# Performance work log

Measured on AMD Instinct MI355X. Metric: run time of the kernel, lower is better.

## Reference

```python
import jax, jax.numpy as jnp
import numpy as np

B, S, D, H = 4, 2048, 1024, 16
DH = D // H  # head dim = 64
MASK_VALUE = -1000000.0


def setup_inputs() -> dict:
    key = jax.random.key(0)
    ks = jax.random.split(key, 8)
    return {
        "key": jax.random.normal(ks[0], (B, S, D), jnp.float32),
        "query": jax.random.normal(ks[1], (B, S, D), jnp.float32),
        "value": jax.random.normal(ks[2], (B, S, D), jnp.float32),
        "valid_lens": jax.random.randint(ks[3], (B,), 0, 2048, jnp.int32),
        # nn.Linear weights stored as [out_features, in_features]
        "Wk": jax.random.normal(ks[4], (D, D), jnp.float32) / np.sqrt(D),
        "Wq": jax.random.normal(ks[5], (D, D), jnp.float32) / np.sqrt(D),
        "Wv": jax.random.normal(ks[6], (D, D), jnp.float32) / np.sqrt(D),
        "Wo": jax.random.normal(ks[7], (D, D), jnp.float32) / np.sqrt(D),
    }


def _split_heads(x):
    # [B, S, D] -> [B, H, S, DH]
    return x.reshape(B, S, H, DH).transpose(0, 2, 1, 3)


def reference(key, query, value, valid_lens, Wk, Wq, Wv, Wo):
    # projections (Linear: x @ W^T, bias=False)
    q = _split_heads(query @ Wq.T)  # [B, H, S, DH]
    k = _split_heads(key @ Wk.T)
    v = _split_heads(value @ Wv.T)

    scale = 1.0 / jnp.sqrt(jnp.asarray(DH, q.dtype))
    scores = jnp.einsum("bhqd,bhkd->bhqk", q, k) * scale  # [B, H, S, S]

    # valid_lens masks the key axis per batch element (same for all heads/queries)
    key_mask = jnp.arange(S) < valid_lens[:, None]  # [B, S]
    scores = jnp.where(key_mask[:, None, None, :], scores, MASK_VALUE)

    attn = jax.nn.softmax(scores, axis=-1)
    out = jnp.einsum("bhqk,bhkd->bhqd", attn, v)  # [B, H, S, DH]
    out = out.transpose(0, 2, 1, 3).reshape(B, S, D)  # concat heads
    return out @ Wo.T
```

## Files before the change

kernel.cpp:

```cpp
#include <hip/hip_runtime.h>
#include <hip/hip_bf16.h>
#include <stdint.h>

typedef __bf16 bf16;
typedef __bf16 bf16x4 __attribute__((ext_vector_type(4)));
typedef __bf16 bf16x8 __attribute__((ext_vector_type(8)));
typedef float f32x4 __attribute__((ext_vector_type(4)));
typedef float f32x8 __attribute__((ext_vector_type(8)));

#define MFMA16 __builtin_amdgcn_mfma_f32_16x16x32_bf16

__device__ __forceinline__ void gload_lds16(void* lds, const void* g) {
  __builtin_amdgcn_global_load_lds(
      (const __attribute__((address_space(1))) unsigned int*)g,
      (__attribute__((address_space(3))) unsigned int*)lds, 16, 0, 0);
}

__global__ __launch_bounds__(256) void cvt3(
    const float* __restrict__ s0, const float* __restrict__ s1,
    const float* __restrict__ s2, bf16* __restrict__ d0,
    bf16* __restrict__ d1, bf16* __restrict__ d2) {
  const float* srcs[3] = {s0, s1, s2};
  bf16* dsts[3] = {d0, d1, d2};
  const float* src = srcs[blockIdx.y];
  bf16* dst = dsts[blockIdx.y];
  int i = (blockIdx.x * 256 + threadIdx.x) * 4;
  f32x4 v = *(const f32x4*)(src + i);
  bf16x4 o;
#pragma unroll
  for (int j = 0; j < 4; j++) o[j] = (bf16)v[j];
  *(bf16x4*)(dst + i) = o;
}

__global__ __launch_bounds__(256) void cvt1(const float* __restrict__ src,
                                            bf16* __restrict__ dst) {
  int i = (blockIdx.x * 256 + threadIdx.x) * 4;
  f32x4 v = *(const f32x4*)(src + i);
  bf16x4 o;
#pragma unroll
  for (int j = 0; j < 4; j++) o[j] = (bf16)v[j];
  *(bf16x4*)(dst + i) = o;
}

__global__ __launch_bounds__(256) void cvt4(const float* __restrict__ w0,
                                            const float* __restrict__ w1,
                                            const float* __restrict__ w2,
                                            const float* __restrict__ w3,
                                            bf16* __restrict__ dst) {
  const float* srcs[4] = {w0, w1, w2, w3};
  const float* src = srcs[blockIdx.y];
  int i = (blockIdx.x * 256 + threadIdx.x) * 4;
  f32x4 v = *(const f32x4*)(src + i);
  bf16x4 o;
#pragma unroll
  for (int j = 0; j < 4; j++) o[j] = (bf16)v[j];
  *(bf16x4*)(dst + (size_t)blockIdx.y * 1048576 + i) = o;
}

__device__ __forceinline__ void xcd_remap(int& m0, int& n0) {
  int id = blockIdx.y * 8 + blockIdx.x;
  int xcd = id & 7;
  int j = id >> 3;
  m0 = (xcd * 8 + (j >> 3)) * 128;
  n0 = (j & 7) * 128;
}

__device__ __forceinline__ void gemm_body(const bf16* __restrict__ A,
                                          const bf16* __restrict__ W,
                                          void* __restrict__ Craw, int mode,
                                          int m0, int n0, bf16* As, bf16* Bs) {
  constexpr int K = 1024;
  const int t = threadIdx.x;
  const int lane = t & 63;
  const int quad = lane >> 4;
  const int m16 = lane & 15;
  const int w = t >> 6;
  const int wm = (w >> 1) * 64;
  const int wn = (w & 1) * 64;

  f32x4 acc[4][4];
#pragma unroll
  for (int i = 0; i < 4; i++)
#pragma unroll
    for (int j = 0; j < 4; j++) acc[i][j] = (f32x4){0.f, 0.f, 0.f, 0.f};

  for (int kt = 0; kt < K / 32; kt++) {
    __syncthreads();
#pragma unroll
    for (int p = 0; p < 2; p++) {
      int idx = p * 256 + t;
      int row = idx >> 2;
      int ce = (idx & 3) * 8;
      gload_lds16(&As[idx * 8], A + (size_t)(m0 + row) * K + kt * 32 + ce);
      gload_lds16(&Bs[idx * 8], W + (size_t)(n0 + row) * K + kt * 32 + ce);
    }
    __syncthreads();

    bf16x8 af[4], bfr[4];
#pragma unroll
    for (int i = 0; i < 4; i++) {
      af[i] = *(const bf16x8*)&As[(wm + i * 16 + m16) * 32 + quad * 8];
      bfr[i] = *(const bf16x8*)&Bs[(wn + i * 16 + m16) * 32 + quad * 8];
    }
#pragma unroll
    for (int i = 0; i < 4; i++)
#pragma unroll
      for (int j = 0; j < 4; j++)
        acc[i][j] = MFMA16(af[i], bfr[j], acc[i][j], 0, 0, 0);
  }

#pragma unroll
  for (int i = 0; i < 4; i++) {
    int rbase = m0 + wm + i * 16 + quad * 4;
#pragma unroll
    for (int j = 0; j < 4; j++) {
      int col = n0 + wn + j * 16 + m16;
#pragma unroll
      for (int r = 0; r < 4; r++) {
        int row = rbase + r;
        if (mode == 0) {
          ((float*)Craw)[(size_t)row * 1024 + col] = acc[i][j][r];
        } else {
          int b = row >> 11, s = row & 2047;
          int h = col >> 6, d = col & 63;
          bf16 v = (bf16)acc[i][j][r];
          if (mode == 1)
            ((bf16*)Craw)[(((size_t)(b * 16 + h)) * 2048 + s) * 64 + d] = v;
          else
            ((bf16*)Craw)[(((size_t)(b * 16 + h)) * 64 + d) * 2048 + s] = v;
        }
      }
    }
  }
}

__global__ __launch_bounds__(256) void gemm_qkv(
    const bf16* __restrict__ xq, const bf16* __restrict__ xk,
    const bf16* __restrict__ xv, const bf16* __restrict__ wb,
    const int* __restrict__ vlen, bf16* __restrict__ qp,
    bf16* __restrict__ kp, bf16* __restrict__ vt) {
  __shared__ bf16 As[128 * 32];
  __shared__ bf16 Bs[128 * 32];
  int m0, n0;
  xcd_remap(m0, n0);
  const int z = blockIdx.z;
  if (z >= 1) {
    int b = m0 >> 11;
    int s0 = m0 & 2047;
    int vl = vlen[b];
    if (vl != 0 && s0 >= vl) return;
  }
  const bf16* A = (z == 0) ? xq : (z == 1) ? xk : xv;
  const bf16* W = wb + (size_t)z * 1048576;
  bf16* C = (z == 0) ? qp : (z == 1) ? kp : vt;
  gemm_body(A, W, C, (z == 2) ? 2 : 1, m0, n0, As, Bs);
}

__global__ __launch_bounds__(256) void gemm_one(const bf16* __restrict__ A,
                                                const bf16* __restrict__ W,
                                                void* __restrict__ Craw,
                                                int mode) {
  __shared__ bf16 As[128 * 32];
  __shared__ bf16 Bs[128 * 32];
  int m0, n0;
  xcd_remap(m0, n0);
  gemm_body(A, W, Craw, mode, m0, n0, As, Bs);
}

template <int AF32, int WF32>
__global__ __launch_bounds__(256) void gemm_bt(const void* __restrict__ Araw,
                                               const void* __restrict__ Wraw,
                                               void* __restrict__ Craw,
                                               int mode) {
  constexpr int K = 1024;
  __shared__ bf16 As[128 * 32];
  __shared__ bf16 Bs[128 * 32];
  const int t = threadIdx.x;
  const int lane = t & 63;
  const int quad = lane >> 4;
  const int m16 = lane & 15;
  const int w = t >> 6;
  const int m0 = blockIdx.y * 128;
  const int n0 = blockIdx.x * 128;
  const int wm = (w >> 1) * 64;
  const int wn = (w & 1) * 64;

  f32x4 acc[4][4];
#pragma unroll
  for (int i = 0; i < 4; i++)
#pragma unroll
    for (int j = 0; j < 4; j++) acc[i][j] = (f32x4){0.f, 0.f, 0.f, 0.f};

  for (int kt = 0; kt < K / 32; kt++) {
    bf16x8 aR[2], bR[2];
#pragma unroll
    for (int p = 0; p < 2; p++) {
      int idx = p * 256 + t;
      int row = idx >> 2;
      int ce = (idx & 3) * 8;
      size_t aoff = (size_t)(m0 + row) * K + kt * 32 + ce;
      size_t boff = (size_t)(n0 + row) * K + kt * 32 + ce;
      if constexpr (AF32) {
        f32x8 av = *(const f32x8*)((const float*)Araw + aoff);
#pragma unroll
        for (int j = 0; j < 8; j++) aR[p][j] = (bf16)av[j];
      } else {
        aR[p] = *(const bf16x8*)((const bf16*)Araw + aoff);
      }
      if constexpr (WF32) {
        f32x8 bv = *(const f32x8*)((const float*)Wraw + boff);
#pragma unroll
        for (int j = 0; j < 8; j++) bR[p][j] = (bf16)bv[j];
      } else {
        bR[p] = *(const bf16x8*)((const bf16*)Wraw + boff);
      }
    }
    __syncthreads();
#pragma unroll
    for (int p = 0; p < 2; p++) {
      int idx = p * 256 + t;
      *(bf16x8*)&As[idx * 8] = aR[p];
      *(bf16x8*)&Bs[idx * 8] = bR[p];
    }
    __syncthreads();

    bf16x8 af[4], bfr[4];
#pragma unroll
    for (int i = 0; i < 4; i++) {
      af[i] = *(const bf16x8*)&As[(wm + i * 16 + m16) * 32 + quad * 8];
      bfr[i] = *(const bf16x8*)&Bs[(wn + i * 16 + m16) * 32 + quad * 8];
    }
#pragma unroll
    for (int i = 0; i < 4; i++)
#pragma unroll
      for (int j = 0; j < 4; j++)
        acc[i][j] = MFMA16(af[i], bfr[j], acc[i][j], 0, 0, 0);
  }

#pragma unroll
  for (int i = 0; i < 4; i++) {
    int rbase = m0 + wm + i * 16 + quad * 4;
#pragma unroll
    for (int j = 0; j < 4; j++) {
      int col = n0 + wn + j * 16 + m16;
#pragma unroll
      for (int r = 0; r < 4; r++) {
        int row = rbase + r;
        if (mode == 0) {
          ((float*)Craw)[(size_t)row * 1024 + col] = acc[i][j][r];
        } else {
          int b = row >> 11, s = row & 2047;
          int h = col >> 6, d = col & 63;
          bf16 v = (bf16)acc[i][j][r];
          if (mode == 1)
            ((bf16*)Craw)[(((size_t)(b * 16 + h)) * 2048 + s) * 64 + d] = v;
          else
            ((bf16*)Craw)[(((size_t)(b * 16 + h)) * 64 + d) * 2048 + s] = v;
        }
      }
    }
  }
}

__global__ __launch_bounds__(256) void attn(const bf16* __restrict__ qp,
                                            const bf16* __restrict__ kp,
                                            const bf16* __restrict__ vt,
                                            const int* __restrict__ vlen,
                                            bf16* __restrict__ ctx) {
  __shared__ bf16 Ks[64 * 64];
  __shared__ bf16 Vs[64 * 64];
  __shared__ bf16 Ps[4 * 32 * 72];

  const int t = threadIdx.x;
  const int lane = t & 63;
  const int quad = lane >> 4;
  const int m16 = lane & 15;
  const int sw = m16 & 7;
  const int w = t >> 6;
  const int bh = blockIdx.y;
  const int qt = blockIdx.x;
  const int b = bh >> 4;
  const int h = bh & 15;
  const int vl = vlen[b];

  const float C1 = 0.18033688f;
  const float C2 = 46.166241f;
  const float mArg = (vl == 0) ? 0.0f : -12800.0f;

  bf16x8 qf[2][2];
#pragma unroll
  for (int a = 0; a < 2; a++) {
    const bf16* qb =
        qp + ((size_t)(bh * 2048 + qt * 128 + w * 32 + a * 16 + m16)) * 64;
    qf[a][0] = *(const bf16x8*)(qb + quad * 8);
    qf[a][1] = *(const bf16x8*)(qb + 32 + quad * 8);
  }

  float rsum[2][4] = {{0.f, 0.f, 0.f, 0.f}, {0.f, 0.f, 0.f, 0.f}};
  f32x4 o[2][4];
#pragma unroll
  for (int a = 0; a < 2; a++)
#pragma unroll
    for (int nt = 0; nt < 4; nt++) o[a][nt] = (f32x4){0.f, 0.f, 0.f, 0.f};

  const int ktEnd = (vl == 0) ? 32 : ((vl + 63) >> 6);

  for (int kt = 0; kt < ktEnd; kt++) {
    __syncthreads();
#pragma unroll
    for (int p = 0; p < 2; p++) {
      int idx = p * 256 + t;
      int row = idx >> 3;
      int gc = (idx & 7) ^ (row & 7);
      gload_lds16(&Ks[idx * 8],
                  &kp[((size_t)(bh * 2048 + kt * 64 + row)) * 64 + gc * 8]);
      gload_lds16(&Vs[idx * 8],
                  &vt[((size_t)(bh * 64 + row)) * 2048 + kt * 64 + gc * 8]);
    }
    __syncthreads();

    f32x4 s[2][4];
#pragma unroll
    for (int a = 0; a < 2; a++)
#pragma unroll
      for (int nt = 0; nt < 4; nt++) s[a][nt] = (f32x4){0.f, 0.f, 0.f, 0.f};
#pragma unroll
    for (int nt = 0; nt < 4; nt++) {
      int key = nt * 16 + m16;
#pragma unroll
      for (int ks = 0; ks < 2; ks++) {
        bf16x8 kf =
            *(const bf16x8*)&Ks[key * 64 + (((ks * 4 + quad) ^ sw) * 8)];
        s[0][nt] = MFMA16(qf[0][ks], kf, s[0][nt], 0, 0, 0);
        s[1][nt] = MFMA16(qf[1][ks], kf, s[1][nt], 0, 0, 0);
      }
    }

#pragma unroll
    for (int nt = 0; nt < 4; nt++) {
      bool masked = (kt * 64 + nt * 16 + m16) >= vl;
#pragma unroll
      for (int a = 0; a < 2; a++)
#pragma unroll
        for (int r = 0; r < 4; r++) {
          float arg = masked ? mArg : (s[a][nt][r] * C1 - C2);
          bf16 pb = (bf16)__builtin_amdgcn_exp2f(arg);
          rsum[a][r] += (float)pb;
          Ps[w * 2304 + (a * 16 + quad * 4 + r) * 72 + nt * 16 + m16] = pb;
        }
    }

#pragma unroll
    for (int ks = 0; ks < 2; ks++) {
      bf16x8 pf0 = *(const bf16x8*)&Ps[w * 2304 + m16 * 72 + ks * 32 + quad * 8];
      bf16x8 pf1 =
          *(const bf16x8*)&Ps[w * 2304 + (16 + m16) * 72 + ks * 32 + quad * 8];
#pragma unroll
      for (int nt = 0; nt < 4; nt++) {
        int dh = nt * 16 + m16;
        bf16x8 vf =
            *(const bf16x8*)&Vs[dh * 64 + (((ks * 4 + quad) ^ sw) * 8)];
        o[0][nt] = MFMA16(pf0, vf, o[0][nt], 0, 0, 0);
        o[1][nt] = MFMA16(pf1, vf, o[1][nt], 0, 0, 0);
      }
    }
  }

#pragma unroll
  for (int off = 1; off < 16; off <<= 1)
#pragma unroll
    for (int a = 0; a < 2; a++)
#pragma unroll
      for (int r = 0; r < 4; r++) rsum[a][r] += __shfl_xor(rsum[a][r], off);
#pragma unroll
  for (int a = 0; a < 2; a++)
#pragma unroll
    for (int r = 0; r < 4; r++) rsum[a][r] = 1.0f / rsum[a][r];

#pragma unroll
  for (int a = 0; a < 2; a++)
#pragma unroll
    for (int nt = 0; nt < 4; nt++) {
      int dh = nt * 16 + m16;
#pragma unroll
      for (int r = 0; r < 4; r++) {
        int srow = qt * 128 + w * 32 + a * 16 + quad * 4 + r;
        ctx[((size_t)(b * 2048 + srow)) * 1024 + h * 64 + dh] =
            (bf16)(o[a][nt][r] * rsum[a][r]);
      }
    }
}

extern "C" void kernel_launch(void* const* d_in, const int* in_sizes, int n_in,
                              void* d_out, int out_size, void* d_ws,
                              size_t ws_size, hipStream_t stream) {
  const float* key = (const float*)d_in[0];
  const float* query = (const float*)d_in[1];
  const float* value = (const float*)d_in[2];
  const int* vlen = (const int*)d_in[3];
  const float* Wk = (const float*)d_in[4];
  const float* Wq = (const float*)d_in[5];
  const float* Wv = (const float*)d_in[6];
  const float* Wo = (const float*)d_in[7];

  const size_t NE = (size_t)4 * 2048 * 1024;
  const size_t WE = 1048576;

  const size_t needA = (6 * NE + 4 * WE) * sizeof(bf16);
  const size_t needB = (5 * NE + 4 * WE) * sizeof(bf16);
  dim3 gg(8, 64), gb(256);

  if (ws_size >= needA) {
    bf16* qp = (bf16*)d_ws;
    bf16* kp = qp + NE;
    bf16* vt = kp + NE;
    bf16* xq = vt + NE;
    bf16* xk = xq + NE;
    bf16* xv = xk + NE;
    bf16* wb = xv + NE;
    bf16* ctx = xq;

    cvt4<<<dim3(1024, 4), gb, 0, stream>>>(Wq, Wk, Wv, Wo, wb);
    cvt3<<<dim3(8192, 3), gb, 0, stream>>>(query, key, value, xq, xk, xv);
    gemm_qkv<<<dim3(8, 64, 3), gb, 0, stream>>>(xq, xk, xv, wb, vlen, qp, kp,
                                                vt);
    attn<<<dim3(16, 64), gb, 0, stream>>>(qp, kp, vt, vlen, ctx);
    gemm_one<<<gg, gb, 0, stream>>>(ctx, wb + 3 * WE, d_out, 0);
  } else if (ws_size >= needB) {
    bf16* qp = (bf16*)d_ws;
    bf16* kp = qp + NE;
    bf16* vt = kp + NE;
    bf16* ctx = vt + NE;
    bf16* xb = ctx + NE;
    bf16* wb = xb + NE;

    cvt4<<<dim3(1024, 4), gb, 0, stream>>>(Wq, Wk, Wv, Wo, wb);
    cvt1<<<8192, gb, 0, stream>>>(query, xb);
    gemm_one<<<gg, gb, 0, stream>>>(xb, wb + 0 * WE, qp, 1);
    cvt1<<<8192, gb, 0, stream>>>(key, xb);
    gemm_one<<<gg, gb, 0, stream>>>(xb, wb + 1 * WE, kp, 1);
    cvt1<<<8192, gb, 0, stream>>>(value, xb);
    gemm_one<<<gg, gb, 0, stream>>>(xb, wb + 2 * WE, vt, 2);
    attn<<<dim3(16, 64), gb, 0, stream>>>(qp, kp, vt, vlen, ctx);
    gemm_one<<<gg, gb, 0, stream>>>(ctx, wb + 3 * WE, d_out, 0);
  } else {
    bf16* qp = (bf16*)d_ws;
    bf16* kp = qp + NE;
    bf16* vt = kp + NE;
    bf16* ctx = vt + NE;
    gemm_bt<1, 1><<<gg, gb, 0, stream>>>(query, Wq, qp, 1);
    gemm_bt<1, 1><<<gg, gb, 0, stream>>>(key, Wk, kp, 1);
    gemm_bt<1, 1><<<gg, gb, 0, stream>>>(value, Wv, vt, 2);
    attn<<<dim3(16, 64), gb, 0, stream>>>(qp, kp, vt, vlen, ctx);
    gemm_bt<0, 1><<<gg, gb, 0, stream>>>(ctx, Wo, d_out, 0);
  }
}
```

Baseline: 335.4 us.

## Fuse fp32-to-bf16 input conversion into QKV GEMM and retile output projection

The separate cvt3 pass over the three activation tensors is removed. The QKV GEMM now loads fp32 activations straight into XOR-swizzled LDS and converts them to bf16 while building MFMA fragments, which saves a full read-write round trip of the inputs. The output projection gets its own kernel with 128x64 tiles, twice as many blocks, and a different XCD remapping that changes which tiles share an XCD. The trade-offs are twice the LDS per block and extra conversion ALU work inside the GEMM inner loop, and the needB fallback path is dropped.

```diff
diff --git a/kernel.cpp b/kernel.cpp
--- a/kernel.cpp
+++ b/kernel.cpp
@@ -14,32 +14,6 @@
   __builtin_amdgcn_global_load_lds(
       (const __attribute__((address_space(1))) unsigned int*)g,
       (__attribute__((address_space(3))) unsigned int*)lds, 16, 0, 0);
-}
-
-__global__ __launch_bounds__(256) void cvt3(
-    const float* __restrict__ s0, const float* __restrict__ s1,
-    const float* __restrict__ s2, bf16* __restrict__ d0,
-    bf16* __restrict__ d1, bf16* __restrict__ d2) {
-  const float* srcs[3] = {s0, s1, s2};
-  bf16* dsts[3] = {d0, d1, d2};
-  const float* src = srcs[blockIdx.y];
-  bf16* dst = dsts[blockIdx.y];
-  int i = (blockIdx.x * 256 + threadIdx.x) * 4;
-  f32x4 v = *(const f32x4*)(src + i);
-  bf16x4 o;
-#pragma unroll
-  for (int j = 0; j < 4; j++) o[j] = (bf16)v[j];
-  *(bf16x4*)(dst + i) = o;
-}
-
-__global__ __launch_bounds__(256) void cvt1(const float* __restrict__ src,
-                                            bf16* __restrict__ dst) {
-  int i = (blockIdx.x * 256 + threadIdx.x) * 4;
-  f32x4 v = *(const f32x4*)(src + i);
-  bf16x4 o;
-#pragma unroll
-  for (int j = 0; j < 4; j++) o[j] = (bf16)v[j];
-  *(bf16x4*)(dst + i) = o;
 }
 
 __global__ __launch_bounds__(256) void cvt4(const float* __restrict__ w0,
@@ -57,19 +31,41 @@
   *(bf16x4*)(dst + (size_t)blockIdx.y * 1048576 + i) = o;
 }
 
-__device__ __forceinline__ void xcd_remap(int& m0, int& n0) {
+__device__ __forceinline__ void remap8(int& m0, int& n0) {
   int id = blockIdx.y * 8 + blockIdx.x;
   int xcd = id & 7;
   int j = id >> 3;
-  m0 = (xcd * 8 + (j >> 3)) * 128;
+  m0 = ((j >> 3) * 8 + xcd) * 128;
   n0 = (j & 7) * 128;
 }
 
-__device__ __forceinline__ void gemm_body(const bf16* __restrict__ A,
-                                          const bf16* __restrict__ W,
-                                          void* __restrict__ Craw, int mode,
-                                          int m0, int n0, bf16* As, bf16* Bs) {
-  constexpr int K = 1024;
+__device__ __forceinline__ void remap16(int& m0, int& n0) {
+  int id = blockIdx.y * 16 + blockIdx.x;
+  int xcd = id & 7;
+  int j = id >> 3;
+  m0 = ((j >> 4) * 8 + xcd) * 128;
+  n0 = (j & 15) * 64;
+}
+
+__global__ __launch_bounds__(256) void gemm_qkv(
+    const float* __restrict__ q, const float* __restrict__ k,
+    const float* __restrict__ v, const bf16* __restrict__ wb,
+    const int* __restrict__ vlen, bf16* __restrict__ qp,
+    bf16* __restrict__ kp, bf16* __restrict__ vt) {
+  __shared__ float Asf[128 * 32];
+  __shared__ bf16 Bs[128 * 32];
+  int m0, n0;
+  remap8(m0, n0);
+  const int z = blockIdx.z;
+  if (z >= 1) {
+    int b = m0 >> 11, s0 = m0 & 2047, vl = vlen[b];
+    if (vl != 0 && s0 >= vl) return;
+  }
+  const float* A = (z == 0) ? q : (z == 1) ? k : v;
+  const bf16* W = wb + (size_t)z * 1048576;
+  bf16* C = (z == 0) ? qp : (z == 1) ? kp : vt;
+  const int mode = (z == 2) ? 2 : 1;
+
   const int t = threadIdx.x;
   const int lane = t & 63;
   const int quad = lane >> 4;
@@ -84,22 +80,40 @@
 #pragma unroll
     for (int j = 0; j < 4; j++) acc[i][j] = (f32x4){0.f, 0.f, 0.f, 0.f};
 
-  for (int kt = 0; kt < K / 32; kt++) {
-    __syncthreads();
+  for (int kt = 0; kt < 32; kt++) {
+    __syncthreads();
+#pragma unroll
+    for (int p = 0; p < 4; p++) {
+      int idx = p * 256 + t;
+      int row = idx >> 3;
+      int gc = (idx & 7) ^ (row & 7);
+      gload_lds16(&Asf[idx * 4],
+                  A + (size_t)(m0 + row) * 1024 + kt * 32 + gc * 4);
+    }
 #pragma unroll
     for (int p = 0; p < 2; p++) {
       int idx = p * 256 + t;
       int row = idx >> 2;
       int ce = (idx & 3) * 8;
-      gload_lds16(&As[idx * 8], A + (size_t)(m0 + row) * K + kt * 32 + ce);
-      gload_lds16(&Bs[idx * 8], W + (size_t)(n0 + row) * K + kt * 32 + ce);
+      gload_lds16(&Bs[idx * 8],
+                  W + (size_t)(n0 + row) * 1024 + kt * 32 + ce);
     }
     __syncthreads();
 
     bf16x8 af[4], bfr[4];
 #pragma unroll
     for (int i = 0; i < 4; i++) {
-      af[i] = *(const bf16x8*)&As[(wm + i * 16 + m16) * 32 + quad * 8];
+      int rr = wm + i * 16 + m16;
+      int e = rr & 7;
+      f32x4 lo = *(const f32x4*)&Asf[rr * 32 + (((2 * quad) ^ e) * 4)];
+      f32x4 hi = *(const f32x4*)&Asf[rr * 32 + (((2 * quad + 1) ^ e) * 4)];
+      bf16x8 a8;
+#pragma unroll
+      for (int j = 0; j < 4; j++) {
+        a8[j] = (bf16)lo[j];
+        a8[4 + j] = (bf16)hi[j];
+      }
+      af[i] = a8;
       bfr[i] = *(const bf16x8*)&Bs[(wn + i * 16 + m16) * 32 + quad * 8];
     }
 #pragma unroll
@@ -118,53 +132,84 @@
 #pragma unroll
       for (int r = 0; r < 4; r++) {
         int row = rbase + r;
-        if (mode == 0) {
-          ((float*)Craw)[(size_t)row * 1024 + col] = acc[i][j][r];
-        } else {
-          int b = row >> 11, s = row & 2047;
-          int h = col >> 6, d = col & 63;
-          bf16 v = (bf16)acc[i][j][r];
-          if (mode == 1)
-            ((bf16*)Craw)[(((size_t)(b * 16 + h)) * 2048 + s) * 64 + d] = v;
-          else
-            ((bf16*)Craw)[(((size_t)(b * 16 + h)) * 64 + d) * 2048 + s] = v;
-        }
-      }
-    }
-  }
-}
-
-__global__ __launch_bounds__(256) void gemm_qkv(
-    const bf16* __restrict__ xq, const bf16* __restrict__ xk,
-    const bf16* __restrict__ xv, const bf16* __restrict__ wb,
-    const int* __restrict__ vlen, bf16* __restrict__ qp,
-    bf16* __restrict__ kp, bf16* __restrict__ vt) {
+        int b = row >> 11, s = row & 2047;
+        int h = col >> 6, d = col & 63;
+        bf16 val = (bf16)acc[i][j][r];
+        if (mode == 1)
+          C[(((size_t)(b * 16 + h)) * 2048 + s) * 64 + d] = val;
+        else
+          C[(((size_t)(b * 16 + h)) * 64 + d) * 2048 + s] = val;
+      }
+    }
+  }
+}
+
+__global__ __launch_bounds__(256) void gemm_out(const bf16* __restrict__ A,
+                                                const bf16* __restrict__ W,
+                                                float* __restrict__ C) {
   __shared__ bf16 As[128 * 32];
-  __shared__ bf16 Bs[128 * 32];
+  __shared__ bf16 Bs[64 * 32];
   int m0, n0;
-  xcd_remap(m0, n0);
-  const int z = blockIdx.z;
-  if (z >= 1) {
-    int b = m0 >> 11;
-    int s0 = m0 & 2047;
-    int vl = vlen[b];
-    if (vl != 0 && s0 >= vl) return;
-  }
-  const bf16* A = (z == 0) ? xq : (z == 1) ? xk : xv;
-  const bf16* W = wb + (size_t)z * 1048576;
-  bf16* C = (z == 0) ? qp : (z == 1) ? kp : vt;
-  gemm_body(A, W, C, (z == 2) ? 2 : 1, m0, n0, As, Bs);
-}
-
-__global__ __launch_bounds__(256) void gemm_one(const bf16* __restrict__ A,
-                                                const bf16* __restrict__ W,
-                                                void* __restrict__ Craw,
-                                                int mode) {
-  __shared__ bf16 As[128 * 32];
-  __shared__ bf16 Bs[128 * 32];
-  int m0, n0;
-  xcd_remap(m0, n0);
-  gemm_body(A, W, Craw, mode, m0, n0, As, Bs);
+  remap16(m0, n0);
+
+  const int t = threadIdx.x;
+  const int lane = t & 63;
+  const int quad = lane >> 4;
+  const int m16 = lane & 15;
+  const int w = t >> 6;
+  const int wm = (w >> 1) * 64;
+  const int wn = (w & 1) * 32;
+
+  f32x4 acc[4][2];
+#pragma unroll
+  for (int i = 0; i < 4; i++)
+#pragma unroll
+    for (int j = 0; j < 2; j++) acc[i][j] = (f32x4){0.f, 0.f, 0.f, 0.f};
+
+  for (int kt = 0; kt < 32; kt++) {
+    __syncthreads();
+#pragma unroll
+    for (int p = 0; p < 2; p++) {
+      int idx = p * 256 + t;
+      int row = idx >> 2;
+      int ce = (idx & 3) * 8;
+      gload_lds16(&As[idx * 8],
+                  A + (size_t)(m0 + row) * 1024 + kt * 32 + ce);
+    }
+    {
+      int idx = t;
+      int row = idx >> 2;
+      int ce = (idx & 3) * 8;
+      gload_lds16(&Bs[idx * 8],
+                  W + (size_t)(n0 + row) * 1024 + kt * 32 + ce);
+    }
+    __syncthreads();
+
+    bf16x8 af[4], bfr[2];
+#pragma unroll
+    for (int i = 0; i < 4; i++)
+      af[i] = *(const bf16x8*)&As[(wm + i * 16 + m16) * 32 + quad * 8];
+#pragma unroll
+    for (int j = 0; j < 2; j++)
+      bfr[j] = *(const bf16x8*)&Bs[(wn + j * 16 + m16) * 32 + quad * 8];
+#pragma unroll
+    for (int i = 0; i < 4; i++)
+#pragma unroll
+      for (int j = 0; j < 2; j++)
+        acc[i][j] = MFMA16(af[i], bfr[j], acc[i][j], 0, 0, 0);
+  }
+
+#pragma unroll
+  for (int i = 0; i < 4; i++) {
+    int rbase = m0 + wm + i * 16 + quad * 4;
+#pragma unroll
+    for (int j = 0; j < 2; j++) {
+      int col = n0 + wn + j * 16 + m16;
+#pragma unroll
+      for (int r = 0; r < 4; r++)
+        C[(size_t)(rbase + r) * 1024 + col] = acc[i][j][r];
+    }
+  }
 }
 
 template <int AF32, int WF32>
@@ -405,49 +450,29 @@
 
   const size_t NE = (size_t)4 * 2048 * 1024;
   const size_t WE = 1048576;
-
-  const size_t needA = (6 * NE + 4 * WE) * sizeof(bf16);
-  const size_t needB = (5 * NE + 4 * WE) * sizeof(bf16);
-  dim3 gg(8, 64), gb(256);
+  dim3 gb(256);
+
+  const size_t needA = (4 * NE + 4 * WE) * sizeof(bf16);
 
   if (ws_size >= needA) {
     bf16* qp = (bf16*)d_ws;
     bf16* kp = qp + NE;
     bf16* vt = kp + NE;
-    bf16* xq = vt + NE;
-    bf16* xk = xq + NE;
-    bf16* xv = xk + NE;
-    bf16* wb = xv + NE;
-    bf16* ctx = xq;
+    bf16* ctx = vt + NE;
+    bf16* wb = ctx + NE;
 
     cvt4<<<dim3(1024, 4), gb, 0, stream>>>(Wq, Wk, Wv, Wo, wb);
-    cvt3<<<dim3(8192, 3), gb, 0, stream>>>(query, key, value, xq, xk, xv);
-    gemm_qkv<<<dim3(8, 64, 3), gb, 0, stream>>>(xq, xk, xv, wb, vlen, qp, kp,
-                                                vt);
+    gemm_qkv<<<dim3(8, 64, 3), gb, 0, stream>>>(query, key, value, wb, vlen,
+                                                qp, kp, vt);
     attn<<<dim3(16, 64), gb, 0, stream>>>(qp, kp, vt, vlen, ctx);
-    gemm_one<<<gg, gb, 0, stream>>>(ctx, wb + 3 * WE, d_out, 0);
-  } else if (ws_size >= needB) {
-    bf16* qp = (bf16*)d_ws;
-    bf16* kp = qp + NE;
-    bf16* vt = kp + NE;
-    bf16* ctx = vt + NE;
-    bf16* xb = ctx + NE;
-    bf16* wb = xb + NE;
-
-    cvt4<<<dim3(1024, 4), gb, 0, stream>>>(Wq, Wk, Wv, Wo, wb);
-    cvt1<<<8192, gb, 0, stream>>>(query, xb);
-    gemm_one<<<gg, gb, 0, stream>>>(xb, wb + 0 * WE, qp, 1);
-    cvt1<<<8192, gb, 0, stream>>>(key, xb);
-    gemm_one<<<gg, gb, 0, stream>>>(xb, wb + 1 * WE, kp, 1);
-    cvt1<<<8192, gb, 0, stream>>>(value, xb);
-    gemm_one<<<gg, gb, 0, stream>>>(xb, wb + 2 * WE, vt, 2);
-    attn<<<dim3(16, 64), gb, 0, stream>>>(qp, kp, vt, vlen, ctx);
-    gemm_one<<<gg, gb, 0, stream>>>(ctx, wb + 3 * WE, d_out, 0);
+    gemm_out<<<dim3(16, 64), gb, 0, stream>>>(ctx, wb + 3 * WE,
+                                              (float*)d_out);
   } else {
     bf16* qp = (bf16*)d_ws;
     bf16* kp = qp + NE;
     bf16* vt = kp + NE;
     bf16* ctx = vt + NE;
+    dim3 gg(8, 64);
     gemm_bt<1, 1><<<gg, gb, 0, stream>>>(query, Wq, qp, 1);
     gemm_bt<1, 1><<<gg, gb, 0, stream>>>(key, Wk, kp, 1);
     gemm_bt<1, 1><<<gg, gb, 0, stream>>>(value, Wv, vt, 2);
```

Measured after the change: 340.9 us. About the same (+1.6%).
